# Optimization experiments

Measured on AMD Instinct MI355X. Metric: run time of the kernel, lower is better.

Reference implementation:

```python
import jax, jax.numpy as jnp
import numpy as np

B = 8_388_608   # batch size
L = 32          # number of tanh-affine layers (1 input layer + 31 hidden layers)
CLIP = 5.0      # clip applied to hidden-layer weights/biases at construction


def setup_inputs() -> dict:
    key = jax.random.key(0)
    ks = jax.random.split(key, 8)
    x = jax.random.normal(ks[0], (B, 2), dtype=jnp.float32)
    # Stacked per-layer params: Linear(2,2) weight/bias, elementwise scale/shift
    W = jax.random.normal(ks[1], (L, 2, 2), dtype=jnp.float32) * 0.5
    b = jax.random.normal(ks[2], (L, 2), dtype=jnp.float32) * 0.1
    scale = jax.random.normal(ks[3], (L, 2), dtype=jnp.float32) * 0.5 + 1.0
    shift = jax.random.normal(ks[4], (L, 2), dtype=jnp.float32) * 0.1
    # clip_weights=True applies only to hidden layers (index >= 1), at construction
    W = W.at[1:].set(jnp.clip(W[1:], -CLIP, CLIP))
    b = b.at[1:].set(jnp.clip(b[1:], -CLIP, CLIP))
    # Final Linear(2,1)
    w_out = jax.random.normal(ks[5], (1, 2), dtype=jnp.float32) * 0.5
    b_out = jax.random.normal(ks[6], (1,), dtype=jnp.float32) * 0.1
    return {"x": x, "W": W, "b": b, "scale": scale, "shift": shift,
            "w_out": w_out, "b_out": b_out}


def reference(x, W, b, scale, shift, w_out, b_out):
    # Sequential chain of L layers: h = tanh(h @ W_l^T + b_l) * scale_l + shift_l
    def step(h, params):
        w_l, b_l, sc_l, sh_l = params
        h = jnp.tanh(h @ w_l.T + b_l) * sc_l + sh_l
        return h, None
    h, _ = jax.lax.scan(step, x, (W, b, scale, shift))
    # Final Linear(2,1)
    return h @ w_out.T + b_out
```

## Files before the change

### kernel.cpp

```cpp
#include <hip/hip_runtime.h>


constexpr int LAYERS = 32;
constexpr int BLOCK  = 256;
constexpr int R4     = 4;

__device__ __forceinline__ float tanh_pre(float zs) {
#if __has_builtin(__builtin_amdgcn_exp2f)
    float e = __builtin_amdgcn_exp2f(zs);
#else
    float e = exp2f(zs);
#endif
#if __has_builtin(__builtin_amdgcn_rcpf)
    float r = __builtin_amdgcn_rcpf(e + 1.0f);
#else
    float r = 1.0f / (e + 1.0f);
#endif
    return fmaf(-2.0f, r, 1.0f);
}

__global__ __launch_bounds__(BLOCK) void fraud_fwd(
        const float* __restrict__ x,
        const float* __restrict__ W,
        const float* __restrict__ b,
        const float* __restrict__ scale,
        const float* __restrict__ shift,
        const float* __restrict__ w_out,
        const float* __restrict__ b_out,
        float* __restrict__ out)
{
    __shared__ float sP[LAYERS * 8];
    __shared__ float sF[4];

    const int t = threadIdx.x;
    const float c = 2.885390081777927f;

    if (t < LAYERS) {
        float w00 = W[t*4+0], w01 = W[t*4+1], w10 = W[t*4+2], w11 = W[t*4+3];
        float b0 = b[t*2+0], b1 = b[t*2+1];
        if (t > 0) {
            float s0  = scale[(t-1)*2+0], s1  = scale[(t-1)*2+1];
            float sh0 = shift[(t-1)*2+0], sh1 = shift[(t-1)*2+1];
            b0 += w00*sh0 + w01*sh1;
            b1 += w10*sh0 + w11*sh1;
            w00 *= s0; w01 *= s1; w10 *= s0; w11 *= s1;
        }
        sP[t*8+0] = w00*c; sP[t*8+1] = w01*c;
        sP[t*8+2] = w10*c; sP[t*8+3] = w11*c;
        sP[t*8+4] = b0 *c; sP[t*8+5] = b1 *c;
        sP[t*8+6] = 0.f;   sP[t*8+7] = 0.f;
    } else if (t == LAYERS) {
        float s0  = scale[31*2+0], s1  = scale[31*2+1];
        float sh0 = shift[31*2+0], sh1 = shift[31*2+1];
        float wo0 = w_out[0], wo1 = w_out[1];
        sF[0] = wo0*s0;
        sF[1] = wo1*s1;
        sF[2] = b_out[0] + wo0*sh0 + wo1*sh1;
        sF[3] = 0.f;
    }
    __syncthreads();

    const float4* __restrict__ xv = (const float4*)x;
    float2*       __restrict__ ov = (float2*)out;
    const int base4 = blockIdx.x * (BLOCK * R4) + t;

    float hx[2*R4], hy[2*R4];
    #pragma unroll
    for (int i = 0; i < R4; ++i) {
        float4 a = xv[base4 + i*BLOCK];
        hx[2*i+0] = a.x; hy[2*i+0] = a.y;
        hx[2*i+1] = a.z; hy[2*i+1] = a.w;
    }

    for (int l = 0; l < LAYERS; ++l) {
        const float4 w  = *(const float4*)&sP[l*8];
        const float b0v = sP[l*8+4];
        const float b1v = sP[l*8+5];
        #pragma unroll
        for (int r = 0; r < 2*R4; ++r) {
            float z0 = fmaf(hx[r], w.x, fmaf(hy[r], w.y, b0v));
            float z1 = fmaf(hx[r], w.z, fmaf(hy[r], w.w, b1v));
            hx[r] = tanh_pre(z0);
            hy[r] = tanh_pre(z1);
        }
    }

    const float wo0 = sF[0], wo1 = sF[1], bo = sF[2];
    #pragma unroll
    for (int i = 0; i < R4; ++i) {
        float2 o;
        o.x = fmaf(hx[2*i+0], wo0, fmaf(hy[2*i+0], wo1, bo));
        o.y = fmaf(hx[2*i+1], wo0, fmaf(hy[2*i+1], wo1, bo));
        ov[base4 + i*BLOCK] = o;
    }
}

extern "C" void kernel_launch(void* const* d_in, const int* in_sizes, int n_in,
                              void* d_out, int out_size, void* d_ws, size_t ws_size,
                              hipStream_t stream) {
    const float* x     = (const float*)d_in[0];
    const float* W     = (const float*)d_in[1];
    const float* b     = (const float*)d_in[2];
    const float* scale = (const float*)d_in[3];
    const float* shift = (const float*)d_in[4];
    const float* w_out = (const float*)d_in[5];
    const float* b_out = (const float*)d_in[6];
    float* out = (float*)d_out;

    const int B = in_sizes[0] / 2;
    const int rows_per_block = BLOCK * R4 * 2;
    const int blocks = B / rows_per_block;

    fraud_fwd<<<blocks, BLOCK, 0, stream>>>(x, W, b, scale, shift, w_out, b_out, out);
}
```

Measured before the change: 198.5 us.

## Share one reciprocal across both tanh lanes via reparameterized sigmoid form

Each hidden state is now carried as g = 1/(e+1), with the tanh affine (1-2g) folded into the next layer's weights and biases on the host-side prep threads. The two reciprocals per layer are merged into a single rcp of d0*d1, giving gx = d1*r and gy = d0*r. This cuts transcendental ops from four to three per row-layer and drops the final fma, at the cost of two extra multiplies. The product d0*d1 can overflow to inf when both exponentials are large, which risks NaN or precision loss. The layer loop is also fully unrolled.

```diff
diff --git a/kernel.cpp b/kernel.cpp
--- a/kernel.cpp
+++ b/kernel.cpp
@@ -5,18 +5,33 @@
 constexpr int BLOCK  = 256;
 constexpr int R4     = 4;
 
-__device__ __forceinline__ float tanh_pre(float zs) {
+__device__ __forceinline__ float fast_exp2(float x) {
 #if __has_builtin(__builtin_amdgcn_exp2f)
-    float e = __builtin_amdgcn_exp2f(zs);
+    return __builtin_amdgcn_exp2f(x);
 #else
-    float e = exp2f(zs);
+    return exp2f(x);
 #endif
+}
+__device__ __forceinline__ float fast_rcp(float x) {
 #if __has_builtin(__builtin_amdgcn_rcpf)
-    float r = __builtin_amdgcn_rcpf(e + 1.0f);
+    return __builtin_amdgcn_rcpf(x);
 #else
-    float r = 1.0f / (e + 1.0f);
+    return 1.0f / x;
 #endif
-    return fmaf(-2.0f, r, 1.0f);
+}
+
+__device__ __forceinline__ void layer_g(float ga, float gb,
+                                        const float4 m, float C0, float C1,
+                                        float& gx, float& gy) {
+    float zs0 = fmaf(ga, m.x, fmaf(gb, m.y, C0));
+    float zs1 = fmaf(ga, m.z, fmaf(gb, m.w, C1));
+    float e0 = fast_exp2(zs0);
+    float e1 = fast_exp2(zs1);
+    float d0 = e0 + 1.0f;
+    float d1 = e1 + 1.0f;
+    float r  = fast_rcp(d0 * d1);
+    gx = d1 * r;
+    gy = d0 * r;
 }
 
 __global__ __launch_bounds__(BLOCK) void fraud_fwd(
@@ -38,24 +53,30 @@
     if (t < LAYERS) {
         float w00 = W[t*4+0], w01 = W[t*4+1], w10 = W[t*4+2], w11 = W[t*4+3];
         float b0 = b[t*2+0], b1 = b[t*2+1];
+        float m00, m01, m10, m11, C0, C1;
         if (t > 0) {
-            float s0  = scale[(t-1)*2+0], s1  = scale[(t-1)*2+1];
-            float sh0 = shift[(t-1)*2+0], sh1 = shift[(t-1)*2+1];
-            b0 += w00*sh0 + w01*sh1;
-            b1 += w10*sh0 + w11*sh1;
-            w00 *= s0; w01 *= s1; w10 *= s0; w11 *= s1;
+            float s0 = scale[(t-1)*2+0], s1 = scale[(t-1)*2+1];
+            float u0 = s0 + shift[(t-1)*2+0], u1 = s1 + shift[(t-1)*2+1];
+            C0 = c * (b0 + w00*u0 + w01*u1);
+            C1 = c * (b1 + w10*u0 + w11*u1);
+            float k = -2.0f * c;
+            m00 = k*w00*s0; m01 = k*w01*s1;
+            m10 = k*w10*s0; m11 = k*w11*s1;
+        } else {
+            C0 = c*b0; C1 = c*b1;
+            m00 = c*w00; m01 = c*w01; m10 = c*w10; m11 = c*w11;
         }
-        sP[t*8+0] = w00*c; sP[t*8+1] = w01*c;
-        sP[t*8+2] = w10*c; sP[t*8+3] = w11*c;
-        sP[t*8+4] = b0 *c; sP[t*8+5] = b1 *c;
-        sP[t*8+6] = 0.f;   sP[t*8+7] = 0.f;
+        sP[t*8+0] = m00; sP[t*8+1] = m01;
+        sP[t*8+2] = m10; sP[t*8+3] = m11;
+        sP[t*8+4] = C0;  sP[t*8+5] = C1;
+        sP[t*8+6] = 0.f; sP[t*8+7] = 0.f;
     } else if (t == LAYERS) {
-        float s0  = scale[31*2+0], s1  = scale[31*2+1];
-        float sh0 = shift[31*2+0], sh1 = shift[31*2+1];
+        float s0 = scale[31*2+0], s1 = scale[31*2+1];
+        float u0 = s0 + shift[31*2+0], u1 = s1 + shift[31*2+1];
         float wo0 = w_out[0], wo1 = w_out[1];
-        sF[0] = wo0*s0;
-        sF[1] = wo1*s1;
-        sF[2] = b_out[0] + wo0*sh0 + wo1*sh1;
+        sF[0] = -2.0f * wo0 * s0;
+        sF[1] = -2.0f * wo1 * s1;
+        sF[2] = b_out[0] + wo0*u0 + wo1*u1;
         sF[3] = 0.f;
     }
     __syncthreads();
@@ -64,33 +85,36 @@
     float2*       __restrict__ ov = (float2*)out;
     const int base4 = blockIdx.x * (BLOCK * R4) + t;
 
-    float hx[2*R4], hy[2*R4];
-    #pragma unroll
-    for (int i = 0; i < R4; ++i) {
-        float4 a = xv[base4 + i*BLOCK];
-        hx[2*i+0] = a.x; hy[2*i+0] = a.y;
-        hx[2*i+1] = a.z; hy[2*i+1] = a.w;
-    }
+    float gx[2*R4], gy[2*R4];
 
-    for (int l = 0; l < LAYERS; ++l) {
-        const float4 w  = *(const float4*)&sP[l*8];
-        const float b0v = sP[l*8+4];
-        const float b1v = sP[l*8+5];
+    {
+        const float4 m0 = *(const float4*)&sP[0];
+        const float C0 = sP[4], C1 = sP[5];
         #pragma unroll
-        for (int r = 0; r < 2*R4; ++r) {
-            float z0 = fmaf(hx[r], w.x, fmaf(hy[r], w.y, b0v));
-            float z1 = fmaf(hx[r], w.z, fmaf(hy[r], w.w, b1v));
-            hx[r] = tanh_pre(z0);
-            hy[r] = tanh_pre(z1);
+        for (int i = 0; i < R4; ++i) {
+            float4 a = xv[base4 + i*BLOCK];
+            layer_g(a.x, a.y, m0, C0, C1, gx[2*i+0], gy[2*i+0]);
+            layer_g(a.z, a.w, m0, C0, C1, gx[2*i+1], gy[2*i+1]);
         }
     }
 
-    const float wo0 = sF[0], wo1 = sF[1], bo = sF[2];
+    #pragma unroll
+    for (int l = 1; l < LAYERS; ++l) {
+        const float4 m  = *(const float4*)&sP[l*8];
+        const float C0 = sP[l*8+4];
+        const float C1 = sP[l*8+5];
+        #pragma unroll
+        for (int r = 0; r < 2*R4; ++r) {
+            layer_g(gx[r], gy[r], m, C0, C1, gx[r], gy[r]);
+        }
+    }
+
+    const float Mo0 = sF[0], Mo1 = sF[1], Co = sF[2];
     #pragma unroll
     for (int i = 0; i < R4; ++i) {
         float2 o;
-        o.x = fmaf(hx[2*i+0], wo0, fmaf(hy[2*i+0], wo1, bo));
-        o.y = fmaf(hx[2*i+1], wo0, fmaf(hy[2*i+1], wo1, bo));
+        o.x = fmaf(gx[2*i+0], Mo0, fmaf(gy[2*i+0], Mo1, Co));
+        o.y = fmaf(gx[2*i+1], Mo0, fmaf(gy[2*i+1], Mo1, Co));
         ov[base4 + i*BLOCK] = o;
     }
 }
```

Result: faster. 193.6 us (-2.4%).
